# Kernel optimization log

Measured on AMD Instinct MI355X. Metric: run time of the kernel, lower is better.

The kernel has to match this reference:

```python
import jax, jax.numpy as jnp
import numpy as np

ALPHA = 0.2  # LeakyReLU negative slope
NEG_INF = -1e9


def setup_inputs() -> dict:
    key = jax.random.key(0)
    k1, k2, k3, k4 = jax.random.split(key, 4)
    B, N, IN, OUT = 8, 2048, 512, 32
    graph_input = jax.random.normal(k1, (B, N, IN), dtype=jnp.float32)
    adj = jax.random.randint(k2, (B, N, N), 0, 2, dtype=jnp.int32)
    W_fc = jax.random.normal(k3, (OUT, IN), dtype=jnp.float32) * (1.0 / np.sqrt(IN))
    W_attn = jax.random.normal(k4, (1, 2 * OUT), dtype=jnp.float32) * (1.0 / np.sqrt(2 * OUT))
    return {"graph_input": graph_input, "adj": adj, "W_fc": W_fc, "W_attn": W_attn}


def reference(graph_input, adj, W_fc, W_attn):
    # h: [B, N, 32]
    h = jnp.einsum('bni,oi->bno', graph_input, W_fc)
    out_dim = W_fc.shape[0]
    # attn_fc(cat(h_i, h_j)) is separable: a1.h_i + a2.h_j
    a1 = W_attn[0, :out_dim]   # [32]
    a2 = W_attn[0, out_dim:]   # [32]
    f1 = jnp.einsum('bno,o->bn', h, a1)  # [B, N]
    f2 = jnp.einsum('bno,o->bn', h, a2)  # [B, N]
    scores = jax.nn.leaky_relu(f1[:, :, None] + f2[:, None, :], negative_slope=ALPHA)  # [B,N,N]
    scores = jnp.where(adj == 0, NEG_INF, scores)
    attn = jax.nn.softmax(scores, axis=2)
    # NOTE: original multiplies attention with graph_input (not h)
    h_prime = jnp.einsum('bnm,bmi->bni', attn, graph_input)  # [B, N, IN]
    return jax.nn.elu(h_prime)  # concat=True path
```

## Files before the change

### kernel.cpp

```cpp
#include <hip/hip_runtime.h>
#include <hip/hip_bf16.h>

#define BATCH 8
#define NN    2048
#define FIN   512
#define FOUT  32
#define GALPHA 0.2f

typedef float  f32x4  __attribute__((ext_vector_type(4)));
typedef __bf16 bf16x8 __attribute__((ext_vector_type(8)));
typedef unsigned short u16;
typedef u16 u16x8 __attribute__((ext_vector_type(8)));

static __device__ __forceinline__ u16 f2bf(float f) {
    __hip_bfloat16 h = __float2bfloat16(f);
    union { __hip_bfloat16 h; u16 u; } c; c.h = h; return c.u;
}
static __device__ __forceinline__ float bf2f(u16 u) {
    union { u16 u; __hip_bfloat16 h; } c; c.u = u; return __bfloat162float(c.h);
}

__global__ void k_w12(const float* __restrict__ Wfc,
                      const float* __restrict__ Wat,
                      float* __restrict__ w1, float* __restrict__ w2) {
    int i = threadIdx.x;
    float s1 = 0.f, s2 = 0.f;
    #pragma unroll
    for (int o = 0; o < FOUT; o++) {
        float wv = Wfc[o * FIN + i];
        s1 += wv * Wat[o];
        s2 += wv * Wat[FOUT + o];
    }
    w1[i] = s1; w2[i] = s2;
}

__global__ void k_f12(const float* __restrict__ x,
                      const float* __restrict__ w1, const float* __restrict__ w2,
                      float* __restrict__ f1, float* __restrict__ f2) {
    int row  = blockIdx.x * 4 + (threadIdx.x >> 6);
    int lane = threadIdx.x & 63;
    const f32x4* xv = (const f32x4*)(x + (size_t)row * FIN + lane * 8);
    f32x4 xa = xv[0], xb = xv[1];
    const f32x4* w1v = (const f32x4*)(w1 + lane * 8);
    const f32x4* w2v = (const f32x4*)(w2 + lane * 8);
    f32x4 wa = w1v[0], wb = w1v[1], wc = w2v[0], wd = w2v[1];
    float s1 = 0.f, s2 = 0.f;
    #pragma unroll
    for (int j = 0; j < 4; j++) {
        s1 += xa[j] * wa[j]; s2 += xa[j] * wc[j];
        s1 += xb[j] * wb[j]; s2 += xb[j] * wd[j];
    }
    #pragma unroll
    for (int off = 32; off; off >>= 1) {
        s1 += __shfl_xor(s1, off);
        s2 += __shfl_xor(s2, off);
    }
    if (lane == 0) { f1[row] = s1; f2[row] = s2; }
}

__global__ void k_xt(const float* __restrict__ x,
                     __hip_bfloat16* __restrict__ xt) {
    int bx = blockIdx.x;
    int it = bx & 7, mt = (bx >> 3) & 31, b = bx >> 8;
    int m0 = mt * 64, i0 = it * 64;
    __shared__ u16 tile[64][72];
    int tt = threadIdx.x;
    int mm = tt >> 3;
    int ic = (tt & 7) * 8;
    const float* xb = x + ((size_t)b * NN + m0) * FIN + i0;
    #pragma unroll
    for (int h = 0; h < 2; h++) {
        int m = mm + h * 32;
        const f32x4* src = (const f32x4*)(xb + (size_t)m * FIN + ic);
        f32x4 v0 = src[0], v1 = src[1];
        u16x8 pk;
        #pragma unroll
        for (int j = 0; j < 4; j++) { pk[j] = f2bf(v0[j]); pk[4 + j] = f2bf(v1[j]); }
        *(u16x8*)&tile[m][ic] = pk;
    }
    __syncthreads();
    __hip_bfloat16* xtb = xt + ((size_t)b * FIN + i0) * NN + m0;
    int mc = (tt & 7) * 8;
    #pragma unroll
    for (int h = 0; h < 2; h++) {
        int ii = (tt >> 3) + h * 32;
        u16x8 v;
        #pragma unroll
        for (int j = 0; j < 8; j++) v[j] = tile[mc + j][ii];
        *(u16x8*)(xtb + (size_t)ii * NN + mc) = v;
    }
}

__global__ __launch_bounds__(512, 2) void k_main(
    const int* __restrict__ adj, const __hip_bfloat16* __restrict__ xt,
    const float* __restrict__ f1, const float* __restrict__ f2,
    float* __restrict__ out)
{
    const int bx = blockIdx.x;
    const int b = bx & 7, rt = bx >> 3;
    const int n0 = rt * 64;
    const int tid = threadIdx.x;
    const int lane = tid & 63, wv = tid >> 6;
    const int quad = lane >> 4, l15 = lane & 15;

    __shared__ u16 At[2][64 * 40];
    __shared__ float rs[64];

    const int grow = tid >> 3;
    const int gch  = (tid & 7) * 4;
    const int*   adjp = adj + ((size_t)b * NN + (n0 + grow)) * NN + gch;
    const float* f2p  = f2 + b * NN + gch;
    const float  f1v  = f1[b * NN + n0 + grow];
    float rpart = 0.f;

    const __hip_bfloat16* xtp = xt + ((size_t)(b * FIN) + wv * 64 + l15) * NN + quad * 8;

    f32x4 acc[4][4];
    #pragma unroll
    for (int s = 0; s < 4; s++)
        #pragma unroll
        for (int c = 0; c < 4; c++)
            acc[s][c] = (f32x4){0.f, 0.f, 0.f, 0.f};

    auto gen = [&](int buf, int4 av, float4 fv) {
        const int*   ai = (const int*)&av;
        const float* fi = (const float*)&fv;
        ushort4 pk;
        u16* pp = (u16*)&pk;
        #pragma unroll
        for (int j = 0; j < 4; j++) {
            float s  = f1v + fi[j];
            float ls = fmaxf(s, GALPHA * s);
            float ev = (ai[j] != 0) ? __expf(ls) : 0.f;
            u16 hb = f2bf(ev);
            rpart += bf2f(hb);
            pp[j] = hb;
        }
        *(ushort4*)&At[buf][grow * 40 + gch] = pk;
    };

    int4   adjv = *(const int4*)adjp;
    float4 f2v  = *(const float4*)f2p;
    bf16x8 Bv[4], Bn[4];
    #pragma unroll
    for (int c = 0; c < 4; c++)
        Bv[c] = *(const bf16x8*)(xtp + (size_t)(c * 16) * NN);
    gen(0, adjv, f2v);
    adjv = *(const int4*)(adjp + 32);
    f2v  = *(const float4*)(f2p + 32);
    __syncthreads();

    #pragma unroll 2
    for (int k = 0; k < 64; k++) {
        const int cur = k & 1;
        if (k < 63) {
            const __hip_bfloat16* xk = xtp + (k + 1) * 32;
            #pragma unroll
            for (int c = 0; c < 4; c++)
                Bn[c] = *(const bf16x8*)(xk + (size_t)(c * 16) * NN);
        }
        #pragma unroll
        for (int s = 0; s < 4; s++) {
            bf16x8 Af = *(const bf16x8*)&At[cur][(s * 16 + l15) * 40 + quad * 8];
            #pragma unroll
            for (int c = 0; c < 4; c++)
                acc[s][c] = __builtin_amdgcn_mfma_f32_16x16x32_bf16(Af, Bv[c], acc[s][c], 0, 0, 0);
        }
        if (k < 63) {
            gen(1 - cur, adjv, f2v);
            if (k < 62) {
                adjv = *(const int4*)(adjp + (size_t)(k + 2) * 32);
                f2v  = *(const float4*)(f2p + (k + 2) * 32);
            }
        }
        asm volatile("s_waitcnt lgkmcnt(0)\ns_barrier" ::: "memory");
        #pragma unroll
        for (int c = 0; c < 4; c++) Bv[c] = Bn[c];
    }

    #pragma unroll
    for (int off = 1; off < 8; off <<= 1) rpart += __shfl_xor(rpart, off);
    if ((tid & 7) == 0) rs[grow] = 1.0f / rpart;
    __syncthreads();

    #pragma unroll
    for (int s = 0; s < 4; s++) {
        #pragma unroll
        for (int r = 0; r < 4; r++) {
            const int row = s * 16 + quad * 4 + r;
            const float inv = rs[row];
            float* op = out + ((size_t)b * NN + (n0 + row)) * FIN + wv * 64 + l15;
            #pragma unroll
            for (int c = 0; c < 4; c++) {
                float v = acc[s][c][r] * inv;
                v = v > 0.f ? v : (__expf(v) - 1.f);
                op[c * 16] = v;
            }
        }
    }
}

extern "C" void kernel_launch(void* const* d_in, const int* in_sizes, int n_in,
                              void* d_out, int out_size, void* d_ws, size_t ws_size,
                              hipStream_t stream) {
    const float* x   = (const float*)d_in[0];
    const int*   adj = (const int*)d_in[1];
    const float* Wfc = (const float*)d_in[2];
    const float* Wat = (const float*)d_in[3];
    float* out = (float*)d_out;

    float* w1 = (float*)d_ws;
    float* w2 = w1 + 512;
    float* f1 = w2 + 512;
    float* f2 = f1 + BATCH * NN;
    __hip_bfloat16* xt = (__hip_bfloat16*)(f2 + BATCH * NN);

    hipLaunchKernelGGL(k_w12, dim3(1),    dim3(512), 0, stream, Wfc, Wat, w1, w2);
    hipLaunchKernelGGL(k_f12, dim3(4096), dim3(256), 0, stream, x, w1, w2, f1, f2);
    hipLaunchKernelGGL(k_xt,  dim3(2048), dim3(256), 0, stream, x, xt);
    hipLaunchKernelGGL(k_main, dim3(256), dim3(512), 0, stream, adj, xt, f1, f2, out);
}
```

Baseline: 298.1 us.

## Fuse f1/f2 into transpose kernel and halve row tile in main kernel

Merges the f1/f2 dot-product kernel into the bf16 transpose kernel, accumulating partial dot products with atomics after a memset, so x is read once instead of twice. The main kernel now uses 32-row tiles with a 64-wide k step, launching 512 blocks instead of 256 to fill more CUs, with occupancy hint raised to 4. It also XOR-swizzles the LDS attention tile to avoid bank conflicts and prefetches adjacency two steps ahead. The trade-off is that each xt element is reloaded by twice as many blocks, and the float atomics make f1/f2 summation order nondeterministic.

New measurement: 341.0 us. 14.4% more time.

```diff
diff --git a/kernel.cpp b/kernel.cpp
--- a/kernel.cpp
+++ b/kernel.cpp
@@ -6,6 +6,8 @@
 #define FIN   512
 #define FOUT  32
 #define GALPHA 0.2f
+#define RT    32
+#define NIT   32
 
 typedef float  f32x4  __attribute__((ext_vector_type(4)));
 typedef __bf16 bf16x8 __attribute__((ext_vector_type(8)));
@@ -34,32 +36,10 @@
     w1[i] = s1; w2[i] = s2;
 }
 
-__global__ void k_f12(const float* __restrict__ x,
+__global__ void k_xtf(const float* __restrict__ x,
                       const float* __restrict__ w1, const float* __restrict__ w2,
+                      __hip_bfloat16* __restrict__ xt,
                       float* __restrict__ f1, float* __restrict__ f2) {
-    int row  = blockIdx.x * 4 + (threadIdx.x >> 6);
-    int lane = threadIdx.x & 63;
-    const f32x4* xv = (const f32x4*)(x + (size_t)row * FIN + lane * 8);
-    f32x4 xa = xv[0], xb = xv[1];
-    const f32x4* w1v = (const f32x4*)(w1 + lane * 8);
-    const f32x4* w2v = (const f32x4*)(w2 + lane * 8);
-    f32x4 wa = w1v[0], wb = w1v[1], wc = w2v[0], wd = w2v[1];
-    float s1 = 0.f, s2 = 0.f;
-    #pragma unroll
-    for (int j = 0; j < 4; j++) {
-        s1 += xa[j] * wa[j]; s2 += xa[j] * wc[j];
-        s1 += xb[j] * wb[j]; s2 += xb[j] * wd[j];
-    }
-    #pragma unroll
-    for (int off = 32; off; off >>= 1) {
-        s1 += __shfl_xor(s1, off);
-        s2 += __shfl_xor(s2, off);
-    }
-    if (lane == 0) { f1[row] = s1; f2[row] = s2; }
-}
-
-__global__ void k_xt(const float* __restrict__ x,
-                     __hip_bfloat16* __restrict__ xt) {
     int bx = blockIdx.x;
     int it = bx & 7, mt = (bx >> 3) & 31, b = bx >> 8;
     int m0 = mt * 64, i0 = it * 64;
@@ -68,15 +48,35 @@
     int mm = tt >> 3;
     int ic = (tt & 7) * 8;
     const float* xb = x + ((size_t)b * NN + m0) * FIN + i0;
+    const f32x4* w1p = (const f32x4*)(w1 + i0 + ic);
+    const f32x4* w2p = (const f32x4*)(w2 + i0 + ic);
+    f32x4 wA = w1p[0], wB = w1p[1], wC = w2p[0], wD = w2p[1];
+    float p1[2], p2[2];
     #pragma unroll
     for (int h = 0; h < 2; h++) {
         int m = mm + h * 32;
         const f32x4* src = (const f32x4*)(xb + (size_t)m * FIN + ic);
         f32x4 v0 = src[0], v1 = src[1];
         u16x8 pk;
-        #pragma unroll
-        for (int j = 0; j < 4; j++) { pk[j] = f2bf(v0[j]); pk[4 + j] = f2bf(v1[j]); }
+        float s1 = 0.f, s2 = 0.f;
+        #pragma unroll
+        for (int j = 0; j < 4; j++) {
+            pk[j] = f2bf(v0[j]); pk[4 + j] = f2bf(v1[j]);
+            s1 += v0[j] * wA[j] + v1[j] * wB[j];
+            s2 += v0[j] * wC[j] + v1[j] * wD[j];
+        }
+        p1[h] = s1; p2[h] = s2;
         *(u16x8*)&tile[m][ic] = pk;
+    }
+    #pragma unroll
+    for (int off = 1; off < 8; off <<= 1) {
+        p1[0] += __shfl_xor(p1[0], off); p1[1] += __shfl_xor(p1[1], off);
+        p2[0] += __shfl_xor(p2[0], off); p2[1] += __shfl_xor(p2[1], off);
+    }
+    if ((tt & 7) == 0) {
+        size_t r0 = (size_t)b * NN + m0 + mm;
+        atomicAdd(&f1[r0], p1[0]);      atomicAdd(&f1[r0 + 32], p1[1]);
+        atomicAdd(&f2[r0], p2[0]);      atomicAdd(&f2[r0 + 32], p2[1]);
     }
     __syncthreads();
     __hip_bfloat16* xtb = xt + ((size_t)b * FIN + i0) * NN + m0;
@@ -91,23 +91,24 @@
     }
 }
 
-__global__ __launch_bounds__(512, 2) void k_main(
+__global__ __launch_bounds__(512, 4) void k_main(
     const int* __restrict__ adj, const __hip_bfloat16* __restrict__ xt,
     const float* __restrict__ f1, const float* __restrict__ f2,
     float* __restrict__ out)
 {
     const int bx = blockIdx.x;
     const int b = bx & 7, rt = bx >> 3;
-    const int n0 = rt * 64;
+    const int n0 = rt * RT;
     const int tid = threadIdx.x;
     const int lane = tid & 63, wv = tid >> 6;
     const int quad = lane >> 4, l15 = lane & 15;
 
-    __shared__ u16 At[2][64 * 40];
-    __shared__ float rs[64];
-
-    const int grow = tid >> 3;
-    const int gch  = (tid & 7) * 4;
+    __shared__ u16 At[2][RT * 64];
+    __shared__ float rs[RT];
+
+    const int grow = tid >> 4;
+    const int gch  = (tid & 15) * 4;
+    const int wofs = grow * 64 + (gch ^ (8 * (grow & 7)));
     const int*   adjp = adj + ((size_t)b * NN + (n0 + grow)) * NN + gch;
     const float* f2p  = f2 + b * NN + gch;
     const float  f1v  = f1[b * NN + n0 + grow];
@@ -115,9 +116,9 @@
 
     const __hip_bfloat16* xtp = xt + ((size_t)(b * FIN) + wv * 64 + l15) * NN + quad * 8;
 
-    f32x4 acc[4][4];
-    #pragma unroll
-    for (int s = 0; s < 4; s++)
+    f32x4 acc[2][4];
+    #pragma unroll
+    for (int s = 0; s < 2; s++)
         #pragma unroll
         for (int c = 0; c < 4; c++)
             acc[s][c] = (f32x4){0.f, 0.f, 0.f, 0.f};
@@ -136,55 +137,63 @@
             rpart += bf2f(hb);
             pp[j] = hb;
         }
-        *(ushort4*)&At[buf][grow * 40 + gch] = pk;
+        *(ushort4*)&At[buf][wofs] = pk;
     };
 
-    int4   adjv = *(const int4*)adjp;
-    float4 f2v  = *(const float4*)f2p;
-    bf16x8 Bv[4], Bn[4];
-    #pragma unroll
-    for (int c = 0; c < 4; c++)
-        Bv[c] = *(const bf16x8*)(xtp + (size_t)(c * 16) * NN);
-    gen(0, adjv, f2v);
-    adjv = *(const int4*)(adjp + 32);
-    f2v  = *(const float4*)(f2p + 32);
+    int4   a0 = *(const int4*)adjp;
+    float4 g0 = *(const float4*)f2p;
+    int4   aring[2];
+    float4 fring[2];
+    gen(0, a0, g0);
+    aring[1] = *(const int4*)(adjp + 64);
+    fring[1] = *(const float4*)(f2p + 64);
+    aring[0] = *(const int4*)(adjp + 128);
+    fring[0] = *(const float4*)(f2p + 128);
     __syncthreads();
 
     #pragma unroll 2
-    for (int k = 0; k < 64; k++) {
-        const int cur = k & 1;
-        if (k < 63) {
-            const __hip_bfloat16* xk = xtp + (k + 1) * 32;
+    for (int t = 0; t < NIT; t++) {
+        const int cur = t & 1;
+        const __hip_bfloat16* xk = xtp + t * 64;
+        bf16x8 B0[4], B1[4];
+        #pragma unroll
+        for (int c = 0; c < 4; c++) {
+            B0[c] = *(const bf16x8*)(xk + (size_t)(c * 16) * NN);
+            B1[c] = *(const bf16x8*)(xk + 32 + (size_t)(c * 16) * NN);
+        }
+        #pragma unroll
+        for (int s = 0; s < 2; s++) {
+            const int rsw = 8 * ((s * 16 + l15) & 7);
+            bf16x8 Af0 = *(const bf16x8*)&At[cur][(s * 16 + l15) * 64 + ((quad * 8) ^ rsw)];
             #pragma unroll
             for (int c = 0; c < 4; c++)
-                Bn[c] = *(const bf16x8*)(xk + (size_t)(c * 16) * NN);
-        }
-        #pragma unroll
-        for (int s = 0; s < 4; s++) {
-            bf16x8 Af = *(const bf16x8*)&At[cur][(s * 16 + l15) * 40 + quad * 8];
+                acc[s][c] = __builtin_amdgcn_mfma_f32_16x16x32_bf16(Af0, B0[c], acc[s][c], 0, 0, 0);
+        }
+        #pragma unroll
+        for (int s = 0; s < 2; s++) {
+            const int rsw = 8 * ((s * 16 + l15) & 7);
+            bf16x8 Af1 = *(const bf16x8*)&At[cur][(s * 16 + l15) * 64 + ((32 + quad * 8) ^ rsw)];
             #pragma unroll
             for (int c = 0; c < 4; c++)
-                acc[s][c] = __builtin_amdgcn_mfma_f32_16x16x32_bf16(Af, Bv[c], acc[s][c], 0, 0, 0);
-        }
-        if (k < 63) {
-            gen(1 - cur, adjv, f2v);
-            if (k < 62) {
-                adjv = *(const int4*)(adjp + (size_t)(k + 2) * 32);
-                f2v  = *(const float4*)(f2p + (k + 2) * 32);
+                acc[s][c] = __builtin_amdgcn_mfma_f32_16x16x32_bf16(Af1, B1[c], acc[s][c], 0, 0, 0);
+        }
+        if (t < NIT - 1) {
+            gen(1 - cur, aring[(t + 1) & 1], fring[(t + 1) & 1]);
+            if (t < NIT - 3) {
+                aring[(t + 1) & 1] = *(const int4*)(adjp + (size_t)(t + 3) * 64);
+                fring[(t + 1) & 1] = *(const float4*)(f2p + (size_t)(t + 3) * 64);
             }
         }
         asm volatile("s_waitcnt lgkmcnt(0)\ns_barrier" ::: "memory");
-        #pragma unroll
-        for (int c = 0; c < 4; c++) Bv[c] = Bn[c];
-    }
-
-    #pragma unroll
-    for (int off = 1; off < 8; off <<= 1) rpart += __shfl_xor(rpart, off);
-    if ((tid & 7) == 0) rs[grow] = 1.0f / rpart;
+    }
+
+    #pragma unroll
+    for (int off = 1; off < 16; off <<= 1) rpart += __shfl_xor(rpart, off);
+    if ((tid & 15) == 0) rs[grow] = 1.0f / rpart;
     __syncthreads();
 
     #pragma unroll
-    for (int s = 0; s < 4; s++) {
+    for (int s = 0; s < 2; s++) {
         #pragma unroll
         for (int r = 0; r < 4; r++) {
             const int row = s * 16 + quad * 4 + r;
@@ -215,8 +224,8 @@
     float* f2 = f1 + BATCH * NN;
     __hip_bfloat16* xt = (__hip_bfloat16*)(f2 + BATCH * NN);
 
+    hipMemsetAsync(f1, 0, (size_t)2 * BATCH * NN * sizeof(float), stream);
     hipLaunchKernelGGL(k_w12, dim3(1),    dim3(512), 0, stream, Wfc, Wat, w1, w2);
-    hipLaunchKernelGGL(k_f12, dim3(4096), dim3(256), 0, stream, x, w1, w2, f1, f2);
-    hipLaunchKernelGGL(k_xt,  dim3(2048), dim3(256), 0, stream, x, xt);
-    hipLaunchKernelGGL(k_main, dim3(256), dim3(512), 0, stream, adj, xt, f1, f2, out);
-}
+    hipLaunchKernelGGL(k_xtf, dim3(2048), dim3(256), 0, stream, x, w1, w2, xt, f1, f2);
+    hipLaunchKernelGGL(k_main, dim3(512), dim3(512), 0, stream, adj, xt, f1, f2, out);
+}
```
